# Optimization experiments

Measured on AMD Instinct MI355X. Metric: run time of the kernel, lower is better.

## Reference

```python
import jax, jax.numpy as jnp
import numpy as np
from jax import lax

DILATIONS = (1, 2, 4, 8)
PADDINGS = (4, 8, 16, 32)  # 2p = 8d -> 'same' length for kernel 9


def setup_inputs() -> dict:
    key = jax.random.key(0)
    ks = jax.random.split(key, 8)
    B, Ci, H, W = 16, 128, 64, 64
    inp = {}
    for i in range(4):
        inp[f"x{i+1}"] = jax.random.normal(ks[i], (B, Ci, H, W), dtype=jnp.float32)
    inp["conv_w"] = jax.random.normal(ks[4], (4, 1, 1, 9), dtype=jnp.float32) * 0.3
    inp["conv_b"] = jax.random.normal(ks[5], (4,), dtype=jnp.float32) * 0.1
    inp["lin_w"] = jax.random.normal(ks[6], (1, 4), dtype=jnp.float32) * 0.5
    inp["lin_b"] = jax.random.normal(ks[7], (1,), dtype=jnp.float32) * 0.1
    return inp


def reference(x1, x2, x3, x4, conv_w, conv_b, lin_w, lin_b):
    # map1: [B, C, H, W] with C = sum of channels
    map1 = jnp.concatenate([x1, x2, x3, x4], axis=1)
    # global average pool -> [B, 1, C] treated as 1D sequence over channels
    gp = jnp.mean(map1, axis=(2, 3))            # [B, C]
    seq = gp[:, None, :]                        # [B, 1, C]
    branch_outs = []
    for i, (d, p) in enumerate(zip(DILATIONS, PADDINGS)):
        o = lax.conv_general_dilated(
            seq, conv_w[i],                     # [B,1,C] x [1,1,9]
            window_strides=(1,),
            padding=[(p, p)],
            rhs_dilation=(d,),
            dimension_numbers=("NCH", "OIH", "NCH"),
        ) + conv_b[i]
        branch_outs.append(o)                   # each [B,1,C]
    cat = jnp.concatenate(branch_outs, axis=1)  # [B,4,C]
    feat = jax.nn.relu(jnp.transpose(cat, (0, 2, 1)))  # [B,C,4]
    lin = jnp.einsum("bcf,of->bco", feat, lin_w) + lin_b  # [B,C,1]
    gate = jax.nn.sigmoid(lin)[..., None]       # [B,C,1,1]
    return gate * map1
```

## Files before the change

### kernel.cpp

```cpp
#include <hip/hip_runtime.h>
#include <math.h>

#define PLANES   8192
#define PLANE_SZ 4096
#define CHANS    512
#define NBLK     4096
#define PPB      2

typedef float f32x4 __attribute__((ext_vector_type(4)));

__global__ __launch_bounds__(256, 4) void fused_kernel(
    const float* __restrict__ x1, const float* __restrict__ x2,
    const float* __restrict__ x3, const float* __restrict__ x4,
    const float* __restrict__ conv_w, const float* __restrict__ conv_b,
    const float* __restrict__ lin_w,  const float* __restrict__ lin_b,
    float* __restrict__ gp, unsigned* __restrict__ flags,
    float* __restrict__ out)
{
    const int tid = threadIdx.x;
    const int blk = blockIdx.x;
    const int bat = blk >> 8;
    const int lb  = blk & 255;
    const int c1  = lb * PPB;
    const int pA  = bat * CHANS + c1;
    const int xi  = c1 >> 7;
    const float* src = (xi == 0) ? x1 : (xi == 1) ? x2 : (xi == 2) ? x3 : x4;
    const f32x4* p4 = (const f32x4*)(src + (size_t)(bat * 128 + (c1 & 127)) * PLANE_SZ);

    __shared__ float gwin[PPB + 64];
    __shared__ float wsum[PPB][4];
    __shared__ float gates[PPB];

    f32x4 v[PPB][4];
    #pragma unroll
    for (int p = 0; p < PPB; ++p)
        #pragma unroll
        for (int j = 0; j < 4; ++j)
            v[p][j] = __builtin_nontemporal_load(&p4[p * 1024 + j * 256 + tid]);

    float s[PPB];
    #pragma unroll
    for (int p = 0; p < PPB; ++p) {
        f32x4 t = (v[p][0] + v[p][1]) + (v[p][2] + v[p][3]);
        s[p] = (t.x + t.y) + (t.z + t.w);
    }
    #pragma unroll
    for (int off = 32; off > 0; off >>= 1)
        #pragma unroll
        for (int p = 0; p < PPB; ++p)
            s[p] += __shfl_down(s[p], off, 64);
    if ((tid & 63) == 0)
        #pragma unroll
        for (int p = 0; p < PPB; ++p)
            wsum[p][tid >> 6] = s[p];
    __syncthreads();

    if (tid < PPB) {
        float m = ((wsum[tid][0] + wsum[tid][1]) +
                   (wsum[tid][2] + wsum[tid][3])) * (1.0f / PLANE_SZ);
        __hip_atomic_store(&gp[pA + tid], m, __ATOMIC_RELAXED, __HIP_MEMORY_SCOPE_AGENT);
    }

    #pragma unroll
    for (int p = 0; p < PPB; ++p)
        #pragma unroll
        for (int j = 0; j < 4; ++j)
            asm volatile("" : "+v"(v[p][j]));

    if (tid == 0) {
        asm volatile("s_waitcnt vmcnt(0)" ::: "memory");
        __hip_atomic_store(&flags[blk * 16], 1u, __ATOMIC_RELAXED, __HIP_MEMORY_SCOPE_AGENT);
    }
    __syncthreads();

    {
        const int lo = (lb - 16 < 0) ? 0 : lb - 16;
        const int hi = (lb + 16 > 255) ? 255 : lb + 16;
        const int nf = hi - lo + 1;
        if (tid < nf) {
            const unsigned* f = &flags[((bat << 8) + lo + tid) * 16];
            while (__hip_atomic_load(f, __ATOMIC_RELAXED, __HIP_MEMORY_SCOPE_AGENT) == 0u)
                __builtin_amdgcn_s_sleep(8);
        }
    }
    __syncthreads();
    asm volatile("" ::: "memory");

    if (tid < PPB + 64) {
        int idx = c1 - 32 + tid;
        gwin[tid] = (idx >= 0 && idx < CHANS)
            ? __hip_atomic_load(&gp[bat * CHANS + idx], __ATOMIC_RELAXED, __HIP_MEMORY_SCOPE_AGENT)
            : 0.f;
    }
    __syncthreads();

    if (tid < PPB) {
        float lin = lin_b[0];
        #pragma unroll
        for (int i = 0; i < 4; ++i) {
            const int d = 1 << i;
            float acc = conv_b[i];
            #pragma unroll
            for (int k = 0; k < 9; ++k)
                acc += conv_w[i * 9 + k] * gwin[32 + tid + d * (k - 4)];
            lin += lin_w[i] * fmaxf(acc, 0.f);
        }
        gates[tid] = 1.0f / (1.0f + expf(-lin));
    }
    __syncthreads();

    f32x4* o4 = (f32x4*)(out + (size_t)pA * PLANE_SZ);
    #pragma unroll
    for (int p = 0; p < PPB; ++p) {
        const float gv = gates[p];
        #pragma unroll
        for (int j = 0; j < 4; ++j) {
            f32x4 t = v[p][j] * gv;
            __builtin_nontemporal_store(t, &o4[p * 1024 + j * 256 + tid]);
        }
    }
}

extern "C" void kernel_launch(void* const* d_in, const int* in_sizes, int n_in,
                              void* d_out, int out_size, void* d_ws, size_t ws_size,
                              hipStream_t stream) {
    const float* x1     = (const float*)d_in[0];
    const float* x2     = (const float*)d_in[1];
    const float* x3     = (const float*)d_in[2];
    const float* x4     = (const float*)d_in[3];
    const float* conv_w = (const float*)d_in[4];
    const float* conv_b = (const float*)d_in[5];
    const float* lin_w  = (const float*)d_in[6];
    const float* lin_b  = (const float*)d_in[7];
    float* out = (float*)d_out;

    float*    gp    = (float*)d_ws;
    unsigned* flags = (unsigned*)((char*)d_ws + PLANES * sizeof(float));

    hipMemsetAsync(flags, 0, NBLK * 16 * sizeof(unsigned), stream);

    fused_kernel<<<NBLK, 256, 0, stream>>>(x1, x2, x3, x4,
                                           conv_w, conv_b, lin_w, lin_b,
                                           gp, flags, out);
}
```

Baseline: 56.76 us.

## Process two batches per block to overlap second load with first gate wait

Halves the grid so each block handles the same channel pair for two batches (b and b+8). It loads and reduces the first batch, publishes its flag, then loads the second batch before spinning on neighbour flags, so the wait and gate compute for batch one overlap with the second batch's loads. This doubles per-thread register-held data, which can lower occupancy, and it relies on all 2048 blocks being co-resident for the spin-wait to stay deadlock-free.

```diff
diff --git a/kernel.cpp b/kernel.cpp
--- a/kernel.cpp
+++ b/kernel.cpp
@@ -4,7 +4,7 @@
 #define PLANES   8192
 #define PLANE_SZ 4096
 #define CHANS    512
-#define NBLK     4096
+#define NBLK     2048
 #define PPB      2
 
 typedef float f32x4 __attribute__((ext_vector_type(4)));
@@ -17,83 +17,121 @@
     float* __restrict__ gp, unsigned* __restrict__ flags,
     float* __restrict__ out)
 {
-    const int tid = threadIdx.x;
-    const int blk = blockIdx.x;
-    const int bat = blk >> 8;
-    const int lb  = blk & 255;
-    const int c1  = lb * PPB;
-    const int pA  = bat * CHANS + c1;
-    const int xi  = c1 >> 7;
-    const float* src = (xi == 0) ? x1 : (xi == 1) ? x2 : (xi == 2) ? x3 : x4;
-    const f32x4* p4 = (const f32x4*)(src + (size_t)(bat * 128 + (c1 & 127)) * PLANE_SZ);
+    const int tid  = threadIdx.x;
+    const int blk  = blockIdx.x;
+    const int bat1 = blk >> 8;
+    const int bat2 = bat1 + 8;
+    const int lb   = blk & 255;
+    const int c1   = lb * PPB;
+    const int pA1  = bat1 * CHANS + c1;
+    const int pA2  = bat2 * CHANS + c1;
+    const int xi   = c1 >> 7;
+    const float* srcb = (xi == 0) ? x1 : (xi == 1) ? x2 : (xi == 2) ? x3 : x4;
+    const f32x4* p4a = (const f32x4*)(srcb + (size_t)(bat1 * 128 + (c1 & 127)) * PLANE_SZ);
+    const f32x4* p4b = (const f32x4*)(srcb + (size_t)(bat2 * 128 + (c1 & 127)) * PLANE_SZ);
 
     __shared__ float gwin[PPB + 64];
-    __shared__ float wsum[PPB][4];
+    __shared__ float wsum1[PPB][4], wsum2[PPB][4];
     __shared__ float gates[PPB];
 
-    f32x4 v[PPB][4];
-    #pragma unroll
-    for (int p = 0; p < PPB; ++p)
-        #pragma unroll
-        for (int j = 0; j < 4; ++j)
-            v[p][j] = __builtin_nontemporal_load(&p4[p * 1024 + j * 256 + tid]);
-
-    float s[PPB];
-    #pragma unroll
-    for (int p = 0; p < PPB; ++p) {
-        f32x4 t = (v[p][0] + v[p][1]) + (v[p][2] + v[p][3]);
-        s[p] = (t.x + t.y) + (t.z + t.w);
-    }
-    #pragma unroll
-    for (int off = 32; off > 0; off >>= 1)
-        #pragma unroll
-        for (int p = 0; p < PPB; ++p)
-            s[p] += __shfl_down(s[p], off, 64);
-    if ((tid & 63) == 0)
-        #pragma unroll
-        for (int p = 0; p < PPB; ++p)
-            wsum[p][tid >> 6] = s[p];
-    __syncthreads();
-
-    if (tid < PPB) {
-        float m = ((wsum[tid][0] + wsum[tid][1]) +
-                   (wsum[tid][2] + wsum[tid][3])) * (1.0f / PLANE_SZ);
-        __hip_atomic_store(&gp[pA + tid], m, __ATOMIC_RELAXED, __HIP_MEMORY_SCOPE_AGENT);
-    }
-
-    #pragma unroll
-    for (int p = 0; p < PPB; ++p)
-        #pragma unroll
-        for (int j = 0; j < 4; ++j)
-            asm volatile("" : "+v"(v[p][j]));
-
+    const int lane = tid & 63, wv = tid >> 6;
+    const int lo = (lb - 16 < 0) ? 0 : lb - 16;
+    const int hi = (lb + 16 > 255) ? 255 : lb + 16;
+    const int base = blk & ~255;
+
+    f32x4 v1[PPB][4];
+    #pragma unroll
+    for (int p = 0; p < PPB; ++p)
+        #pragma unroll
+        for (int j = 0; j < 4; ++j)
+            v1[p][j] = __builtin_nontemporal_load(&p4a[p * 1024 + j * 256 + tid]);
+    {
+        float s[PPB];
+        #pragma unroll
+        for (int p = 0; p < PPB; ++p) {
+            f32x4 t = (v1[p][0] + v1[p][1]) + (v1[p][2] + v1[p][3]);
+            s[p] = (t.x + t.y) + (t.z + t.w);
+        }
+        #pragma unroll
+        for (int off = 32; off > 0; off >>= 1)
+            #pragma unroll
+            for (int p = 0; p < PPB; ++p)
+                s[p] += __shfl_down(s[p], off, 64);
+        if (lane == 0)
+            #pragma unroll
+            for (int p = 0; p < PPB; ++p)
+                wsum1[p][wv] = s[p];
+    }
+    __syncthreads();
+    if (tid < PPB) {
+        float m = ((wsum1[tid][0] + wsum1[tid][1]) +
+                   (wsum1[tid][2] + wsum1[tid][3])) * (1.0f / PLANE_SZ);
+        __hip_atomic_store(&gp[pA1 + tid], m, __ATOMIC_RELAXED, __HIP_MEMORY_SCOPE_AGENT);
+    }
+    #pragma unroll
+    for (int p = 0; p < PPB; ++p)
+        #pragma unroll
+        for (int j = 0; j < 4; ++j)
+            asm volatile("" : "+v"(v1[p][j]));
     if (tid == 0) {
         asm volatile("s_waitcnt vmcnt(0)" ::: "memory");
         __hip_atomic_store(&flags[blk * 16], 1u, __ATOMIC_RELAXED, __HIP_MEMORY_SCOPE_AGENT);
     }
-    __syncthreads();
-
-    {
-        const int lo = (lb - 16 < 0) ? 0 : lb - 16;
-        const int hi = (lb + 16 > 255) ? 255 : lb + 16;
-        const int nf = hi - lo + 1;
-        if (tid < nf) {
-            const unsigned* f = &flags[((bat << 8) + lo + tid) * 16];
-            while (__hip_atomic_load(f, __ATOMIC_RELAXED, __HIP_MEMORY_SCOPE_AGENT) == 0u)
-                __builtin_amdgcn_s_sleep(8);
-        }
+
+    f32x4 v2[PPB][4];
+    #pragma unroll
+    for (int p = 0; p < PPB; ++p)
+        #pragma unroll
+        for (int j = 0; j < 4; ++j)
+            v2[p][j] = __builtin_nontemporal_load(&p4b[p * 1024 + j * 256 + tid]);
+    {
+        float s[PPB];
+        #pragma unroll
+        for (int p = 0; p < PPB; ++p) {
+            f32x4 t = (v2[p][0] + v2[p][1]) + (v2[p][2] + v2[p][3]);
+            s[p] = (t.x + t.y) + (t.z + t.w);
+        }
+        #pragma unroll
+        for (int off = 32; off > 0; off >>= 1)
+            #pragma unroll
+            for (int p = 0; p < PPB; ++p)
+                s[p] += __shfl_down(s[p], off, 64);
+        if (lane == 0)
+            #pragma unroll
+            for (int p = 0; p < PPB; ++p)
+                wsum2[p][wv] = s[p];
+    }
+    __syncthreads();
+    if (tid < PPB) {
+        float m = ((wsum2[tid][0] + wsum2[tid][1]) +
+                   (wsum2[tid][2] + wsum2[tid][3])) * (1.0f / PLANE_SZ);
+        __hip_atomic_store(&gp[pA2 + tid], m, __ATOMIC_RELAXED, __HIP_MEMORY_SCOPE_AGENT);
+    }
+    #pragma unroll
+    for (int p = 0; p < PPB; ++p)
+        #pragma unroll
+        for (int j = 0; j < 4; ++j)
+            asm volatile("" : "+v"(v2[p][j]));
+    if (tid == 0) {
+        asm volatile("s_waitcnt vmcnt(0)" ::: "memory");
+        __hip_atomic_store(&flags[blk * 16 + 4], 1u, __ATOMIC_RELAXED, __HIP_MEMORY_SCOPE_AGENT);
+    }
+    __syncthreads();
+
+    if (tid <= hi - lo) {
+        const unsigned* f = &flags[(base + lo + tid) * 16];
+        while (__hip_atomic_load(f, __ATOMIC_RELAXED, __HIP_MEMORY_SCOPE_AGENT) == 0u)
+            __builtin_amdgcn_s_sleep(8);
     }
     __syncthreads();
     asm volatile("" ::: "memory");
-
     if (tid < PPB + 64) {
         int idx = c1 - 32 + tid;
         gwin[tid] = (idx >= 0 && idx < CHANS)
-            ? __hip_atomic_load(&gp[bat * CHANS + idx], __ATOMIC_RELAXED, __HIP_MEMORY_SCOPE_AGENT)
+            ? __hip_atomic_load(&gp[bat1 * CHANS + idx], __ATOMIC_RELAXED, __HIP_MEMORY_SCOPE_AGENT)
             : 0.f;
     }
     __syncthreads();
-
     if (tid < PPB) {
         float lin = lin_b[0];
         #pragma unroll
@@ -108,15 +146,58 @@
         gates[tid] = 1.0f / (1.0f + expf(-lin));
     }
     __syncthreads();
-
-    f32x4* o4 = (f32x4*)(out + (size_t)pA * PLANE_SZ);
-    #pragma unroll
-    for (int p = 0; p < PPB; ++p) {
-        const float gv = gates[p];
-        #pragma unroll
-        for (int j = 0; j < 4; ++j) {
-            f32x4 t = v[p][j] * gv;
-            __builtin_nontemporal_store(t, &o4[p * 1024 + j * 256 + tid]);
+    {
+        f32x4* o4 = (f32x4*)(out + (size_t)pA1 * PLANE_SZ);
+        #pragma unroll
+        for (int p = 0; p < PPB; ++p) {
+            const float gv = gates[p];
+            #pragma unroll
+            for (int j = 0; j < 4; ++j) {
+                f32x4 t = v1[p][j] * gv;
+                __builtin_nontemporal_store(t, &o4[p * 1024 + j * 256 + tid]);
+            }
+        }
+    }
+    __syncthreads();
+
+    if (tid <= hi - lo) {
+        const unsigned* f = &flags[(base + lo + tid) * 16 + 4];
+        while (__hip_atomic_load(f, __ATOMIC_RELAXED, __HIP_MEMORY_SCOPE_AGENT) == 0u)
+            __builtin_amdgcn_s_sleep(8);
+    }
+    __syncthreads();
+    asm volatile("" ::: "memory");
+    if (tid < PPB + 64) {
+        int idx = c1 - 32 + tid;
+        gwin[tid] = (idx >= 0 && idx < CHANS)
+            ? __hip_atomic_load(&gp[bat2 * CHANS + idx], __ATOMIC_RELAXED, __HIP_MEMORY_SCOPE_AGENT)
+            : 0.f;
+    }
+    __syncthreads();
+    if (tid < PPB) {
+        float lin = lin_b[0];
+        #pragma unroll
+        for (int i = 0; i < 4; ++i) {
+            const int d = 1 << i;
+            float acc = conv_b[i];
+            #pragma unroll
+            for (int k = 0; k < 9; ++k)
+                acc += conv_w[i * 9 + k] * gwin[32 + tid + d * (k - 4)];
+            lin += lin_w[i] * fmaxf(acc, 0.f);
+        }
+        gates[tid] = 1.0f / (1.0f + expf(-lin));
+    }
+    __syncthreads();
+    {
+        f32x4* o4 = (f32x4*)(out + (size_t)pA2 * PLANE_SZ);
+        #pragma unroll
+        for (int p = 0; p < PPB; ++p) {
+            const float gv = gates[p];
+            #pragma unroll
+            for (int j = 0; j < 4; ++j) {
+                f32x4 t = v2[p][j] * gv;
+                __builtin_nontemporal_store(t, &o4[p * 1024 + j * 256 + tid]);
+            }
         }
     }
 }
```

Result: no change. 55.87 us (-1.6%).
